# Performance work log

Measured on AMD Instinct MI355X. Metric: run time of the kernel, lower is better.

The kernel has to match this reference:

```python
import jax, jax.numpy as jnp
import numpy as np

B, S, D, H = 4, 2048, 256, 8
HD = D // H
SCALE = float(np.sqrt(HD))  # temperature = head_dim ** 0.5


def setup_inputs() -> dict:
    key = jax.random.key(0)
    ks = jax.random.split(key, 12)
    w = lambda k, shape: jax.random.normal(k, shape, dtype=jnp.float32) * 0.05
    x = jax.random.normal(ks[0], (B, S, D), dtype=jnp.float32)
    adj = jax.random.randint(ks[1], (B, S, S), 0, 2, dtype=jnp.int32)
    return {
        "x": x,
        "adj": adj,
        "w_qkv": w(ks[2], (3 * D, D)),
        "b_qkv": jnp.zeros((3 * D,), jnp.float32),
        "ln_g": jnp.ones((D,), jnp.float32),
        "ln_b": jnp.zeros((D,), jnp.float32),
        "w_fc": w(ks[3], (D, D)),
        "b_fc": jnp.zeros((D,), jnp.float32),
        "w_z": w(ks[4], (D, D)),
        "b_z": jnp.full((D,), -2.0, jnp.float32),  # init_bias fills w_z bias with -2
        "u_z": w(ks[5], (D, D)),
        "w_r": w(ks[6], (D, D)),
        "u_r": w(ks[7], (D, D)),
        "w_g": w(ks[8], (D, D)),
        "u_g": w(ks[9], (D, D)),
    }


def reference(x, adj, w_qkv, b_qkv, ln_g, ln_b, w_fc, b_fc,
              w_z, b_z, u_z, w_r, u_r, w_g, u_g):
    residual = x
    # LayerNorm (eps=1e-5, torch default)
    mu = jnp.mean(x, axis=-1, keepdims=True)
    var = jnp.var(x, axis=-1, keepdims=True)
    xn = (x - mu) / jnp.sqrt(var + 1e-5) * ln_g + ln_b
    # fused QKV projection -> (B*H, S, 3*HD), batch-major over (b, h)
    qkv = xn @ w_qkv.T + b_qkv                       # [B,S,3D]
    qkv = qkv.reshape(B, S, H, 3 * HD).transpose(0, 2, 1, 3).reshape(B * H, S, 3 * HD)
    q, k, v = jnp.split(qkv, 3, axis=-1)
    # masked scaled dot-product attention (full NxN scores, as in original)
    attn = jnp.einsum('nqd,nkd->nqk', q, k) / SCALE  # [B*H,S,S]
    adj_r = jnp.repeat(adj, H, axis=0)               # batch-major, matches attn layout
    attn = jnp.where(adj_r == 0, -jnp.inf, attn)
    attn = jax.nn.softmax(attn, axis=-1)
    out = jnp.einsum('nqk,nkd->nqd', attn, v)        # [B*H,S,HD]
    # Faithful replication of torch's view(n_head, batch, ...) applied to
    # batch-major data (an ordering quirk in the original module).
    out = out.reshape(H, B, S, HD).transpose(1, 2, 0, 3).reshape(B, S, D)
    y = jax.nn.relu(out @ w_fc.T + b_fc)
    # GRU gate: x=residual, y=attention branch
    z = jax.nn.sigmoid(y @ w_z.T + b_z + residual @ u_z.T)
    r = jax.nn.sigmoid(y @ w_r.T + residual @ u_r.T)
    h_hat = jnp.tanh(y @ w_g.T + (r * residual) @ u_g.T)
    return (1.0 - z) * residual + z * h_hat
```

## Files before the change

### kernel.cpp

```cpp
#include <hip/hip_runtime.h>
#include <hip/hip_bf16.h>
#include <math.h>

#define B_  4
#define S_  2048
#define D_  256
#define H_  8
#define HD_ 32
#define QSCALE 0.25504175929589786f

typedef short  bf16x8 __attribute__((ext_vector_type(8)));
typedef float  f32x4  __attribute__((ext_vector_type(4)));
typedef float  f32x16 __attribute__((ext_vector_type(16)));
typedef unsigned short ushort_t;
typedef unsigned int   uint_t;

__device__ __forceinline__ ushort_t f2b(float f) {
    union { float f; unsigned u; } v; v.f = f;
    unsigned r = (v.u + 0x7FFFu + ((v.u >> 16) & 1u)) >> 16;
    return (ushort_t)r;
}
__device__ __forceinline__ float b2f(ushort_t s) {
    return __uint_as_float((uint_t)s << 16);
}
__device__ __forceinline__ f32x16 zero16() {
    f32x16 z;
#pragma unroll
    for (int i = 0; i < 16; ++i) z[i] = 0.f;
    return z;
}
__device__ __forceinline__ float wave_allsum(float v) {
#pragma unroll
    for (int o = 32; o > 0; o >>= 1) v += __shfl_xor(v, o, 64);
    return v;
}

#define WQ_SZ 196608
#define WS_SZ 65536
#define NB_WQ  48
#define NB_LN4 2048
__global__ __launch_bounds__(256)
void prep_kernel(const float* __restrict__ w0, ushort_t* __restrict__ wout,
                 const float* __restrict__ x, const float* __restrict__ g,
                 const float* __restrict__ bb, ushort_t* __restrict__ xn_b) {
    __shared__ float T[16][260];
    int blk = blockIdx.x, tid = threadIdx.x;
    if (blk < NB_WQ) {
        int ct = blk;
#pragma unroll
        for (int p = 0; p < 4; ++p) {
            int u = p * 256 + tid;
            int row = u >> 6, col = (u & 63) * 4;
            float4 v = *(const float4*)(w0 + (size_t)(ct * 16 + row) * 256 + col);
            T[row][col]     = v.x; T[row][col + 1] = v.y;
            T[row][col + 2] = v.z; T[row][col + 3] = v.w;
        }
        __syncthreads();
        ushort_t* ob = wout + (size_t)blk * 4096;
#pragma unroll
        for (int p = 0; p < 2; ++p) {
            int m = p * 256 + tid;
            int l = m & 15, qd = (m >> 4) & 3, ks = m >> 6;
            const float* tp = &T[l][ks * 32 + qd * 8];
            union { ushort_t u[8]; uint4 q; } pk;
#pragma unroll
            for (int j = 0; j < 8; ++j) pk.u[j] = f2b(tp[j]);
            *(uint4*)(ob + ks * 512 + qd * 128 + l * 8) = pk.q;
        }
    } else {
        int wave = tid >> 6, lane = tid & 63;
        int row = (blk - NB_WQ) * 4 + wave;
        int col = lane * 4;
        float4 t = *(const float4*)(x + (size_t)row * 256 + col);
        float s = wave_allsum(t.x + t.y + t.z + t.w);
        float mu = s * (1.0f / D_);
        float d0 = t.x - mu, d1 = t.y - mu, d2 = t.z - mu, d3 = t.w - mu;
        float v = wave_allsum(d0 * d0 + d1 * d1 + d2 * d2 + d3 * d3);
        float rstd = rsqrtf(v * (1.0f / D_) + 1e-5f);
        float4 gv = *(const float4*)(g + col);
        float4 bv = *(const float4*)(bb + col);
        union { ushort_t u[4]; uint2 q; } o;
        o.u[0] = f2b(d0 * rstd * gv.x + bv.x);
        o.u[1] = f2b(d1 * rstd * gv.y + bv.y);
        o.u[2] = f2b(d2 * rstd * gv.z + bv.z);
        o.u[3] = f2b(d3 * rstd * gv.w + bv.w);
        *(uint2*)(xn_b + (size_t)row * 256 + col) = o.q;
    }
}

__global__ __launch_bounds__(256)
void gemm_qkv(const ushort_t* __restrict__ A, const ushort_t* __restrict__ Wf,
              const float* __restrict__ bias, ushort_t* __restrict__ outb,
              ushort_t* __restrict__ vT, ushort_t* __restrict__ kD,
              const int* __restrict__ adj, uint_t* __restrict__ bits) {
    __shared__ ushort_t Sa[64][264];
    int tid = threadIdx.x;
    int bid = blockIdx.x;
    int grp = bid / 19, r = bid - grp * 19;
    if (r >= 3) {
        int a = grp * 16 + (r - 3);
        int b = a >> 11, q = a & 2047;
        const int4* arow = (const int4*)(adj + (size_t)a * 2048);
        int4 v0 = arow[tid * 2];
        int4 v1 = arow[tid * 2 + 1];
        unsigned byte = (unsigned)(v0.x != 0)        | ((unsigned)(v0.y != 0) << 1)
                      | ((unsigned)(v0.z != 0) << 2) | ((unsigned)(v0.w != 0) << 3)
                      | ((unsigned)(v1.x != 0) << 4) | ((unsigned)(v1.y != 0) << 5)
                      | ((unsigned)(v1.z != 0) << 6) | ((unsigned)(v1.w != 0) << 7);
        unsigned char* lb = (unsigned char*)&Sa[0][0];
        lb[tid] = (unsigned char)byte;
        __syncthreads();
        if (tid < 64) {
            uint_t w = *(const uint_t*)&lb[tid * 4];
            bits[((size_t)b * 64 + tid) * 2048 + q] = w;
        }
        return;
    }
    int gidx = grp * 3 + r;
    int m0 = (gidx / 12) * 64, n0 = (gidx % 12) * 64;

    int wave = tid >> 6, lane = tid & 63, l = lane & 15, quad = lane >> 4;
    int wm = wave >> 1, wn = wave & 1;
    {
#pragma unroll
        for (int j = 0; j < 8; ++j) {
            int u = tid + j * 256;
            int row = u >> 5, c = (u & 31) * 8;
            *(uint4*)&Sa[row][c] = *(const uint4*)(A + (size_t)(m0 + row) * 256 + c);
        }
    }
    __syncthreads();

    bf16x8 af[2][8];
#pragma unroll
    for (int mt = 0; mt < 2; ++mt)
#pragma unroll
        for (int ks = 0; ks < 8; ++ks)
            af[mt][ks] = *(const bf16x8*)&Sa[wm * 32 + mt * 16 + l][ks * 32 + quad * 8];

    f32x4 acc[2][2];
#pragma unroll
    for (int i = 0; i < 2; ++i)
#pragma unroll
        for (int j = 0; j < 2; ++j) acc[i][j] = (f32x4){0.f, 0.f, 0.f, 0.f};

#pragma unroll
    for (int nt = 0; nt < 2; ++nt) {
        int ct = (n0 >> 4) + wn * 2 + nt;
        bf16x8 wfr[8];
#pragma unroll
        for (int ks = 0; ks < 8; ++ks)
            wfr[ks] = *(const bf16x8*)(Wf + (((size_t)ct * 8 + ks) * 64 + lane) * 8);
#pragma unroll
        for (int ks = 0; ks < 8; ++ks) {
            acc[0][nt] = __builtin_amdgcn_mfma_f32_16x16x32_bf16(af[0][ks], wfr[ks], acc[0][nt], 0, 0, 0);
            acc[1][nt] = __builtin_amdgcn_mfma_f32_16x16x32_bf16(af[1][ks], wfr[ks], acc[1][nt], 0, 0, 0);
        }
    }

    __syncthreads();
    ushort_t* So = &Sa[0][0];
#pragma unroll
    for (int nt = 0; nt < 2; ++nt) {
        int col = wn * 32 + nt * 16 + l;
        int gcol = n0 + col;
        float bv = bias[gcol];
        float qs = ((gcol % 96) < 32) ? QSCALE : 1.0f;
#pragma unroll
        for (int mt = 0; mt < 2; ++mt)
#pragma unroll
            for (int r2 = 0; r2 < 4; ++r2) {
                int row = wm * 32 + mt * 16 + quad * 4 + r2;
                So[row * 72 + col] = f2b((acc[mt][nt][r2] + bv) * qs);
            }
    }
    __syncthreads();
    {
        int row = tid >> 2, seg = tid & 3;
        uint4 v0 = *(uint4*)&So[row * 72 + seg * 16];
        uint4 v1 = *(uint4*)&So[row * 72 + seg * 16 + 8];
        ushort_t* op = outb + (size_t)(m0 + row) * 768 + n0 + seg * 16;
        ((uint4*)op)[0] = v0;
        ((uint4*)op)[1] = v1;
    }

    int vs = n0 % 96;

    if (vs != 64) {
        int kloc = (vs == 0) ? 32 : 0;
        int h  = (vs == 0) ? (n0 / 96) : ((n0 - 32) / 96);
        int b  = m0 >> 11;
        int s0 = m0 & (S_ - 1);
        int krow = tid >> 2, kd = (tid & 3) * 8;
        uint4 v = *(uint4*)&So[krow * 72 + kloc + kd];
        *(uint4*)&kD[((size_t)(b * 8 + h) * S_ + s0 + krow) * 32 + kd] = v;
    }

    if (vs != 0) {
        int vloc = (vs == 64) ? 0 : 32;
        int h  = (n0 + vloc) / 96;
        int b  = m0 >> 11;
        int s0 = m0 & (S_ - 1);
        ushort_t* vstage = &Sa[0][0] + 8192;
        {
            int c = tid & 31, seg = tid >> 5;
            ushort_t tmp[8];
#pragma unroll
            for (int i = 0; i < 8; ++i)
                tmp[i] = So[(seg * 8 + i) * 72 + vloc + c];
            uint_t u[4];
#pragma unroll
            for (int i = 0; i < 4; ++i)
                u[i] = (uint_t)tmp[2 * i] | ((uint_t)tmp[2 * i + 1] << 16);
            *(uint4*)&vstage[c * 72 + seg * 8] = make_uint4(u[0], u[1], u[2], u[3]);
        }
        __syncthreads();
        {
            int d = tid >> 3, tseg = tid & 7;
            uint4 v = *(uint4*)&vstage[d * 72 + tseg * 8];
            *(uint4*)&vT[((size_t)(b * 8 + h) * 32 + d) * S_ + s0 + tseg * 8] = v;
        }
    }
}

__global__ __launch_bounds__(512)
void fused_gate(const ushort_t* __restrict__ attn_b, const float* __restrict__ xf,
                const ushort_t* __restrict__ wfc, const ushort_t* __restrict__ wz,
                const ushort_t* __restrict__ uz, const ushort_t* __restrict__ wr,
                const ushort_t* __restrict__ ur, const ushort_t* __restrict__ wg,
                const ushort_t* __restrict__ ug, const float* __restrict__ bfc,
                const float* __restrict__ bz, float* __restrict__ out) {
    __shared__ ushort_t Sa[32][264];
    __shared__ ushort_t Sx[32][264];
    __shared__ ushort_t Sy[32][264];
    auto St = Sa;
    int tid = threadIdx.x;
    int wave = tid >> 6, lane = tid & 63, l = lane & 15, quad = lane >> 4;
    int m0 = blockIdx.x * 32;
    int colbase = wave * 32;

    {
        int row = tid >> 4, c0 = (tid & 15) * 16;
        const ushort_t* ap = attn_b + (size_t)(m0 + row) * 256 + c0;
        uint4 a0 = ((const uint4*)ap)[0];
        uint4 a1 = ((const uint4*)ap)[1];
        *(uint4*)&Sa[row][c0] = a0;
        *(uint4*)&Sa[row][c0 + 8] = a1;
        const float4* xp = (const float4*)(xf + (size_t)(m0 + row) * 256 + c0);
        float4 f0 = xp[0], f1 = xp[1], f2_ = xp[2], f3 = xp[3];
        union { __hip_bfloat162 h[4]; uint4 u; } p0, p1;
        p0.h[0] = __float22bfloat162_rn(make_float2(f0.x, f0.y));
        p0.h[1] = __float22bfloat162_rn(make_float2(f0.z, f0.w));
        p0.h[2] = __float22bfloat162_rn(make_float2(f1.x, f1.y));
        p0.h[3] = __float22bfloat162_rn(make_float2(f1.z, f1.w));
        p1.h[0] = __float22bfloat162_rn(make_float2(f2_.x, f2_.y));
        p1.h[1] = __float22bfloat162_rn(make_float2(f2_.z, f2_.w));
        p1.h[2] = __float22bfloat162_rn(make_float2(f3.x, f3.y));
        p1.h[3] = __float22bfloat162_rn(make_float2(f3.z, f3.w));
        *(uint4*)&Sx[row][c0]     = p0.u;
        *(uint4*)&Sx[row][c0 + 8] = p1.u;
    }
    __syncthreads();

    {
        f32x4 ya[2][2];
#pragma unroll
        for (int mt = 0; mt < 2; ++mt)
#pragma unroll
            for (int nt = 0; nt < 2; ++nt) ya[mt][nt] = (f32x4){0.f, 0.f, 0.f, 0.f};
#pragma unroll
        for (int nt = 0; nt < 2; ++nt) {
            size_t fb = ((size_t)(wave * 2 + nt) * 8) * 512 + lane * 8;
#pragma unroll
            for (int ks = 0; ks < 8; ++ks) {
                bf16x8 wfr = *(const bf16x8*)(wfc + fb + ks * 512);
                bf16x8 a0 = *(const bf16x8*)&Sa[l][ks * 32 + quad * 8];
                bf16x8 a1 = *(const bf16x8*)&Sa[16 + l][ks * 32 + quad * 8];
                ya[0][nt] = __builtin_amdgcn_mfma_f32_16x16x32_bf16(a0, wfr, ya[0][nt], 0, 0, 0);
                ya[1][nt] = __builtin_amdgcn_mfma_f32_16x16x32_bf16(a1, wfr, ya[1][nt], 0, 0, 0);
            }
        }
        __syncthreads();
#pragma unroll
        for (int nt = 0; nt < 2; ++nt) {
            int col = colbase + nt * 16 + l;
            float bv = bfc[col];
#pragma unroll
            for (int mt = 0; mt < 2; ++mt)
#pragma unroll
                for (int r = 0; r < 4; ++r)
                    Sy[mt * 16 + quad * 4 + r][col] = f2b(fmaxf(ya[mt][nt][r] + bv, 0.0f));
        }
    }
    __syncthreads();

    f32x4 az[2][2], ar[2][2], ag[2][2];
#pragma unroll
    for (int mt = 0; mt < 2; ++mt)
#pragma unroll
        for (int nt = 0; nt < 2; ++nt) {
            az[mt][nt] = (f32x4){0.f, 0.f, 0.f, 0.f};
            ar[mt][nt] = (f32x4){0.f, 0.f, 0.f, 0.f};
            ag[mt][nt] = (f32x4){0.f, 0.f, 0.f, 0.f};
        }
#pragma unroll
    for (int nt = 0; nt < 2; ++nt) {
        size_t fb = ((size_t)(wave * 2 + nt) * 8) * 512 + lane * 8;
#pragma unroll
        for (int ks = 0; ks < 8; ++ks) {
            bf16x8 fz  = *(const bf16x8*)(wz + fb + ks * 512);
            bf16x8 fuz = *(const bf16x8*)(uz + fb + ks * 512);
            bf16x8 fr  = *(const bf16x8*)(wr + fb + ks * 512);
            bf16x8 fur = *(const bf16x8*)(ur + fb + ks * 512);
            bf16x8 fg  = *(const bf16x8*)(wg + fb + ks * 512);
            bf16x8 fy0 = *(const bf16x8*)&Sy[l][ks * 32 + quad * 8];
            bf16x8 fy1 = *(const bf16x8*)&Sy[16 + l][ks * 32 + quad * 8];
            bf16x8 fx0 = *(const bf16x8*)&Sx[l][ks * 32 + quad * 8];
            bf16x8 fx1 = *(const bf16x8*)&Sx[16 + l][ks * 32 + quad * 8];
            az[0][nt] = __builtin_amdgcn_mfma_f32_16x16x32_bf16(fy0, fz,  az[0][nt], 0, 0, 0);
            az[0][nt] = __builtin_amdgcn_mfma_f32_16x16x32_bf16(fx0, fuz, az[0][nt], 0, 0, 0);
            az[1][nt] = __builtin_amdgcn_mfma_f32_16x16x32_bf16(fy1, fz,  az[1][nt], 0, 0, 0);
            az[1][nt] = __builtin_amdgcn_mfma_f32_16x16x32_bf16(fx1, fuz, az[1][nt], 0, 0, 0);
            ar[0][nt] = __builtin_amdgcn_mfma_f32_16x16x32_bf16(fy0, fr,  ar[0][nt], 0, 0, 0);
            ar[0][nt] = __builtin_amdgcn_mfma_f32_16x16x32_bf16(fx0, fur, ar[0][nt], 0, 0, 0);
            ar[1][nt] = __builtin_amdgcn_mfma_f32_16x16x32_bf16(fy1, fr,  ar[1][nt], 0, 0, 0);
            ar[1][nt] = __builtin_amdgcn_mfma_f32_16x16x32_bf16(fx1, fur, ar[1][nt], 0, 0, 0);
            ag[0][nt] = __builtin_amdgcn_mfma_f32_16x16x32_bf16(fy0, fg,  ag[0][nt], 0, 0, 0);
            ag[1][nt] = __builtin_amdgcn_mfma_f32_16x16x32_bf16(fy1, fg,  ag[1][nt], 0, 0, 0);
        }
    }
#pragma unroll
    for (int nt = 0; nt < 2; ++nt) {
        int col = colbase + nt * 16 + l;
        float bzv = bz[col];
#pragma unroll
        for (int mt = 0; mt < 2; ++mt)
#pragma unroll
            for (int r = 0; r < 4; ++r) {
                int row = mt * 16 + quad * 4 + r;
                az[mt][nt][r] = 1.0f / (1.0f + __expf(-(az[mt][nt][r] + bzv)));
                float rr  = 1.0f / (1.0f + __expf(-ar[mt][nt][r]));
                St[row][col] = f2b(rr * b2f(Sx[row][col]));
            }
    }
    __syncthreads();

    f32x4 fcc[2][2];
#pragma unroll
    for (int mt = 0; mt < 2; ++mt)
#pragma unroll
        for (int nt = 0; nt < 2; ++nt) fcc[mt][nt] = (f32x4){0.f, 0.f, 0.f, 0.f};
#pragma unroll
    for (int nt = 0; nt < 2; ++nt) {
        size_t fb = ((size_t)(wave * 2 + nt) * 8) * 512 + lane * 8;
#pragma unroll
        for (int ks = 0; ks < 8; ++ks) {
            bf16x8 fu  = *(const bf16x8*)(ug + fb + ks * 512);
            bf16x8 ft0 = *(const bf16x8*)&St[l][ks * 32 + quad * 8];
            bf16x8 ft1 = *(const bf16x8*)&St[16 + l][ks * 32 + quad * 8];
            fcc[0][nt] = __builtin_amdgcn_mfma_f32_16x16x32_bf16(ft0, fu, fcc[0][nt], 0, 0, 0);
            fcc[1][nt] = __builtin_amdgcn_mfma_f32_16x16x32_bf16(ft1, fu, fcc[1][nt], 0, 0, 0);
        }
    }
#pragma unroll
    for (int nt = 0; nt < 2; ++nt) {
        int col = colbase + nt * 16 + l;
#pragma unroll
        for (int mt = 0; mt < 2; ++mt)
#pragma unroll
            for (int r = 0; r < 4; ++r) {
                int row = mt * 16 + quad * 4 + r;
                float v = ag[mt][nt][r] + fcc[mt][nt][r];
                float e = __expf(2.0f * v);
                float h = 1.0f - 2.0f / (e + 1.0f);
                float zz = az[mt][nt][r];
                size_t idx = (size_t)(m0 + row) * 256 + col;
                out[idx] = (1.0f - zz) * xf[idx] + zz * h;
            }
    }
}

#define ATTN_COMPUTE(CUR, A0, A1)                                                         \
    {                                                                                     \
        _Pragma("unroll")                                                                 \
        for (int kb2 = 0; kb2 < 2; ++kb2) {                                               \
            const int kb = kofs + kb2 * 32;                                               \
            bf16x8 kf1 = *(const bf16x8*)&Ks[CUR][kb + lane5][(hi ^ b3) * 8];             \
            bf16x8 kf2 = *(const bf16x8*)&Ks[CUR][kb + lane5][((2 + hi) ^ b3) * 8];       \
            f32x16 sc = zero16();                                                         \
            sc = __builtin_amdgcn_mfma_f32_32x32x16_bf16(kf1, qf1, sc, 0, 0, 0);          \
            sc = __builtin_amdgcn_mfma_f32_32x32x16_bf16(kf2, qf2, sc, 0, 0, 0);          \
            uint_t wsub = (kb2 ? (A1) : (A0)) >> hsh8;                                    \
            union { uint_t u[8]; bf16x8 v[2]; } pp;                                       \
            _Pragma("unroll")                                                             \
            for (int i = 0; i < 8; ++i) {                                                 \
                const int c = 2 * i + ((i >> 2) * 8);                                     \
                float e0 = __builtin_amdgcn_exp2f(sc[2 * i]);                             \
                float e1 = __builtin_amdgcn_exp2f(sc[2 * i + 1]);                         \
                uint_t mm0 = (uint_t)((int)(wsub << (31 - c)) >> 31);                     \
                uint_t mm1 = (uint_t)((int)(wsub << (30 - c)) >> 31);                     \
                e0 = __uint_as_float(__float_as_uint(e0) & mm0);                          \
                e1 = __uint_as_float(__float_as_uint(e1) & mm1);                          \
                union { __hip_bfloat162 b2; uint_t u; } p;                                \
                p.b2 = __float22bfloat162_rn(make_float2(e0, e1));                        \
                pp.u[i] = p.u;                                                            \
            }                                                                             \
            bf16x8 vb1 = *(const bf16x8*)&Vt[CUR][lane5][kb + hsh8];                      \
            bf16x8 vb2 = *(const bf16x8*)&Vt[CUR][lane5][kb + 16 + hsh8];                 \
            __builtin_amdgcn_s_setprio(1);                                                \
            oacc  = __builtin_amdgcn_mfma_f32_32x32x16_bf16(pp.v[0], vb1,  oacc,  0, 0, 0); \
            aones = __builtin_amdgcn_mfma_f32_32x32x16_bf16(pp.v[0], ones, aones, 0, 0, 0); \
            oacc  = __builtin_amdgcn_mfma_f32_32x32x16_bf16(pp.v[1], vb2,  oacc,  0, 0, 0); \
            aones = __builtin_amdgcn_mfma_f32_32x32x16_bf16(pp.v[1], ones, aones, 0, 0, 0); \
            __builtin_amdgcn_s_setprio(0);                                                \
        }                                                                                 \
    }

__global__ __launch_bounds__(256)
void attn_kernel(const ushort_t* __restrict__ qkvb, const ushort_t* __restrict__ kD,
                 const ushort_t* __restrict__ vT,
                 const uint_t* __restrict__ abits, ushort_t* __restrict__ attn_b,
                 const float* __restrict__ gw0, const float* __restrict__ gw1,
                 const float* __restrict__ gw2, const float* __restrict__ gw3,
                 const float* __restrict__ gw4, const float* __restrict__ gw5,
                 const float* __restrict__ gw6, ushort_t* __restrict__ wout) {
    __shared__ ushort_t Ks[2][128][40];
    __shared__ ushort_t Vt[2][32][136];

    int tid = threadIdx.x;
    int lid = blockIdx.x;

    if (lid >= 1024) {
        int wblk = lid - 1024;
        int seg = wblk >> 4, ct = wblk & 15;
        const float* src = (seg == 0) ? gw0 : (seg == 1) ? gw1 : (seg == 2) ? gw2 :
                           (seg == 3) ? gw3 : (seg == 4) ? gw4 : (seg == 5) ? gw5 : gw6;
        float* T = (float*)&Ks[0][0][0];
#pragma unroll
        for (int p = 0; p < 4; ++p) {
            int u = p * 256 + tid;
            int row = u >> 6, col = (u & 63) * 4;
            float4 v = *(const float4*)(src + (size_t)(ct * 16 + row) * 256 + col);
            T[row * 260 + col]     = v.x; T[row * 260 + col + 1] = v.y;
            T[row * 260 + col + 2] = v.z; T[row * 260 + col + 3] = v.w;
        }
        __syncthreads();
        ushort_t* ob = wout + (size_t)(48 + wblk) * 4096;
#pragma unroll
        for (int p = 0; p < 2; ++p) {
            int m = p * 256 + tid;
            int l2 = m & 15, qd = (m >> 4) & 3, ks2 = m >> 6;
            const float* tp = &T[l2 * 260 + ks2 * 32 + qd * 8];
            union { ushort_t u[8]; uint4 q; } pk;
#pragma unroll
            for (int j = 0; j < 8; ++j) pk.u[j] = f2b(tp[j]);
            *(uint4*)(ob + ks2 * 512 + qd * 128 + l2 * 8) = pk.q;
        }
        return;
    }

    int wave = tid >> 6, lane = tid & 63;
    int lane5 = lane & 31, hi = lane >> 5;
    int hsh8 = hi * 8;
    int pair = wave >> 1, half = wave & 1;

    int L   = (lid & 7) * 128 + (lid >> 3);
    int q0  = (L & 31) * 64;
    int n   = L >> 5;
    int b = n >> 3, h = n & 7;
    int bp = n & 3, hp = n >> 2;

    const ushort_t* base = qkvb + (size_t)b * S_ * 768 + h * 96;
    int qbase = pair * 32;
    int myq = q0 + qbase + lane5;
    const int kofs = half * 64;

    bf16x8 qf1 = *(const bf16x8*)(base + (size_t)myq * 768 + hsh8);
    bf16x8 qf2 = *(const bf16x8*)(base + (size_t)myq * 768 + 16 + hsh8);

    bf16x8 ones;
#pragma unroll
    for (int i = 0; i < 8; ++i) ones[i] = (short)0x3F80;

    f32x16 oacc = zero16(), aones = zero16();

    int skey = tid >> 1, sj = tid & 1;
    int prow = (skey & ~12) | ((skey & 4) << 1) | ((skey & 8) >> 1);
    int pxor = ((prow >> 3) & 1) << 3;
    int vd = tid >> 3, vk = (tid & 7) * 8;
    const ushort_t* vptr = vT + ((size_t)n * 32 + vd) * S_ + vk;
    const ushort_t* kpt  = kD + ((size_t)n * S_ + skey) * 32 + sj * 16;
    const uint_t* tb = abits + ((size_t)b * 64) * 2048 + myq;

    uint_t aw0 = tb[(size_t)(half * 2 + 0) * 2048];
    uint_t aw1 = tb[(size_t)(half * 2 + 1) * 2048];
    {
        uint4 ka = *(const uint4*)(kpt);
        uint4 kb_ = *(const uint4*)(kpt + 8);
        uint4 va = *(const uint4*)(vptr);
        uint4 vb_ = *(const uint4*)(vptr + 64);
        *(uint4*)&Ks[0][prow][(sj * 16 + 0) ^ pxor] = ka;
        *(uint4*)&Ks[0][prow][(sj * 16 + 8) ^ pxor] = kb_;
        *(uint4*)&Vt[0][vd][vk] = va;
        *(uint4*)&Vt[0][vd][vk + 64] = vb_;
    }
    uint4 kv0 = *(const uint4*)(kpt + (size_t)128 * 32);
    uint4 kv1 = *(const uint4*)(kpt + (size_t)128 * 32 + 8);
    uint4 vv0 = *(const uint4*)(vptr + 128);
    uint4 vv1 = *(const uint4*)(vptr + 192);
    __syncthreads();

    int b3 = (lane >> 3) & 1;

#pragma unroll 1
    for (int w = 0; w < 15; ++w) {
        int k0 = w * 128;
        int cur = w & 1;
        *(uint4*)&Ks[cur ^ 1][prow][(sj * 16 + 0) ^ pxor] = kv0;
        *(uint4*)&Ks[cur ^ 1][prow][(sj * 16 + 8) ^ pxor] = kv1;
        *(uint4*)&Vt[cur ^ 1][vd][vk] = vv0;
        *(uint4*)&Vt[cur ^ 1][vd][vk + 64] = vv1;
        int wn = ((k0 + 128) >> 5) + half * 2;
        uint_t awn0 = tb[(size_t)(wn + 0) * 2048];
        uint_t awn1 = tb[(size_t)(wn + 1) * 2048];
        int kpre = (k0 + 256) & (S_ - 1);
        kv0 = *(const uint4*)(kpt + (size_t)kpre * 32);
        kv1 = *(const uint4*)(kpt + (size_t)kpre * 32 + 8);
        vv0 = *(const uint4*)(vptr + kpre);
        vv1 = *(const uint4*)(vptr + kpre + 64);

        ATTN_COMPUTE(cur, aw0, aw1)

        aw0 = awn0; aw1 = awn1;
        __syncthreads();
    }
    ATTN_COMPUTE(1, aw0, aw1)
    __syncthreads();

    float* red = (float*)&Ks[0][0][0];
    if (half) {
        float* dst = red + pair * 2048 + lane * 4;
#pragma unroll
        for (int j = 0; j < 4; ++j) {
            f32x4 t;
            t[0] = oacc[4 * j]; t[1] = oacc[4 * j + 1];
            t[2] = oacc[4 * j + 2]; t[3] = oacc[4 * j + 3];
            *(f32x4*)(dst + j * 256) = t;
        }
#pragma unroll
        for (int j = 0; j < 4; ++j) {
            f32x4 t;
            t[0] = aones[4 * j]; t[1] = aones[4 * j + 1];
            t[2] = aones[4 * j + 2]; t[3] = aones[4 * j + 3];
            *(f32x4*)(dst + (4 + j) * 256) = t;
        }
    }
    __syncthreads();
    if (!half) {
        const float* src = red + pair * 2048 + lane * 4;
#pragma unroll
        for (int j = 0; j < 4; ++j) {
            f32x4 t = *(const f32x4*)(src + j * 256);
            oacc[4 * j] += t[0]; oacc[4 * j + 1] += t[1];
            oacc[4 * j + 2] += t[2]; oacc[4 * j + 3] += t[3];
        }
#pragma unroll
        for (int j = 0; j < 4; ++j) {
            f32x4 t = *(const f32x4*)(src + (4 + j) * 256);
            aones[4 * j] += t[0]; aones[4 * j + 1] += t[1];
            aones[4 * j + 2] += t[2]; aones[4 * j + 3] += t[3];
        }
    }
    __syncthreads();

    ushort_t* Ost = &Ks[0][0][0];
    if (!half) {
#pragma unroll
        for (int r = 0; r < 16; ++r) {
            int qr = (r & 3) + 8 * (r >> 2) + 4 * hi;
            Ost[(qbase + qr) * 40 + lane5] = f2b(oacc[r] / aones[r]);
        }
    }
    __syncthreads();
    {
        int row = tid >> 2, part = tid & 3;
        uint4 v = *(uint4*)&Ost[row * 40 + part * 8];
        *(uint4*)&attn_b[((size_t)(bp * S_ + q0 + row)) * 256 + hp * 32 + part * 8] = v;
    }
}

extern "C" void kernel_launch(void* const* d_in, const int* in_sizes, int n_in,
                              void* d_out, int out_size, void* d_ws, size_t ws_size,
                              hipStream_t stream) {
    const float* x     = (const float*)d_in[0];
    const int*   adj   = (const int*)d_in[1];
    const float* w_qkv = (const float*)d_in[2];
    const float* b_qkv = (const float*)d_in[3];
    const float* ln_g  = (const float*)d_in[4];
    const float* ln_b  = (const float*)d_in[5];
    const float* w_fc  = (const float*)d_in[6];
    const float* b_fc  = (const float*)d_in[7];
    const float* w_z   = (const float*)d_in[8];
    const float* b_z   = (const float*)d_in[9];
    const float* u_z   = (const float*)d_in[10];
    const float* w_r   = (const float*)d_in[11];
    const float* u_r   = (const float*)d_in[12];
    const float* w_g   = (const float*)d_in[13];
    const float* u_g   = (const float*)d_in[14];
    float* out = (float*)d_out;

    const size_t TOK  = (size_t)B_ * S_;
    const size_t TOKD = TOK * D_;
    ushort_t* xn_b   = (ushort_t*)d_ws;
    ushort_t* qkv_b  = xn_b + TOKD;
    ushort_t* attn_b = qkv_b + TOK * 768;
    ushort_t* wb     = attn_b + TOKD;
    uint_t*   bits   = (uint_t*)(wb + WQ_SZ + 7 * WS_SZ);
    ushort_t* vTb    = (ushort_t*)(bits + (size_t)B_ * S_ * S_ / 32);
    ushort_t* kDb    = vTb + (size_t)32 * 32 * S_;

    ushort_t* wq_b  = wb;
    ushort_t* wfc_b = wb + WQ_SZ;
    ushort_t* wz_b  = wfc_b + WS_SZ;
    ushort_t* uz_b  = wz_b + WS_SZ;
    ushort_t* wr_b  = uz_b + WS_SZ;
    ushort_t* ur_b  = wr_b + WS_SZ;
    ushort_t* wg_b  = ur_b + WS_SZ;
    ushort_t* ug_b  = wg_b + WS_SZ;

    prep_kernel<<<NB_WQ + NB_LN4, 256, 0, stream>>>(
        w_qkv, wb, x, ln_g, ln_b, xn_b);

    gemm_qkv<<<9728, 256, 0, stream>>>(xn_b, wq_b, b_qkv, qkv_b, vTb, kDb, adj, bits);

    attn_kernel<<<1136, 256, 0, stream>>>(qkv_b, kDb, vTb, bits, attn_b,
                                          w_fc, w_z, u_z, w_r, u_r, w_g, u_g, wb);

    fused_gate<<<256, 512, 0, stream>>>(
        attn_b, x, wfc_b, wz_b, uz_b, wr_b, ur_b, wg_b, ug_b, b_fc, b_z, out);
}
```

Before: 208.7 us.

## Batch adj bit-packing per block and widen fused_gate to 16 waves

Adjacency packing blocks in the QKV GEMM launch now each handle 64 query rows instead of one. They transpose the packed bytes through shared memory and write coalesced uint4 words, which shrinks the grid from 9728 to 1664 blocks and cuts per-block overhead. fused_gate goes from 512 to 1024 threads, with each wave owning one 16-column tile instead of two, so there is more parallelism across the 256 blocks. The risks are lower per-wave ILP, higher register pressure at 1024 threads, and fewer, longer-running packing blocks.

```diff
diff --git a/kernel.cpp b/kernel.cpp
--- a/kernel.cpp
+++ b/kernel.cpp
@@ -96,27 +96,38 @@
     __shared__ ushort_t Sa[64][264];
     int tid = threadIdx.x;
     int bid = blockIdx.x;
-    int grp = bid / 19, r = bid - grp * 19;
-    if (r >= 3) {
-        int a = grp * 16 + (r - 3);
-        int b = a >> 11, q = a & 2047;
-        const int4* arow = (const int4*)(adj + (size_t)a * 2048);
-        int4 v0 = arow[tid * 2];
-        int4 v1 = arow[tid * 2 + 1];
-        unsigned byte = (unsigned)(v0.x != 0)        | ((unsigned)(v0.y != 0) << 1)
-                      | ((unsigned)(v0.z != 0) << 2) | ((unsigned)(v0.w != 0) << 3)
-                      | ((unsigned)(v1.x != 0) << 4) | ((unsigned)(v1.y != 0) << 5)
-                      | ((unsigned)(v1.z != 0) << 6) | ((unsigned)(v1.w != 0) << 7);
+    int grp = bid / 13, r = bid - grp * 13;
+    if (r == 12) {
+        int a = grp;
+        int ab = a >> 5, q0 = (a & 31) * 64;
         unsigned char* lb = (unsigned char*)&Sa[0][0];
-        lb[tid] = (unsigned char)byte;
+#pragma unroll 4
+        for (int rr = 0; rr < 64; ++rr) {
+            const int4* p = (const int4*)(adj + ((size_t)ab * 2048 + q0 + rr) * 2048);
+            int4 v0 = p[tid * 2];
+            int4 v1 = p[tid * 2 + 1];
+            unsigned byte = (unsigned)(v0.x != 0)        | ((unsigned)(v0.y != 0) << 1)
+                          | ((unsigned)(v0.z != 0) << 2) | ((unsigned)(v0.w != 0) << 3)
+                          | ((unsigned)(v1.x != 0) << 4) | ((unsigned)(v1.y != 0) << 5)
+                          | ((unsigned)(v1.z != 0) << 6) | ((unsigned)(v1.w != 0) << 7);
+            lb[rr * 260 + tid] = (unsigned char)byte;
+        }
         __syncthreads();
-        if (tid < 64) {
-            uint_t w = *(const uint_t*)&lb[tid * 4];
-            bits[((size_t)b * 64 + tid) * 2048 + q] = w;
+        {
+            int w = tid >> 2, qq = (tid & 3) * 16;
+            uint_t wd[16];
+#pragma unroll
+            for (int j = 0; j < 16; ++j)
+                wd[j] = *(const uint_t*)&lb[(qq + j) * 260 + w * 4];
+            uint_t* dst = bits + ((size_t)ab * 64 + w) * 2048 + q0 + qq;
+#pragma unroll
+            for (int c = 0; c < 4; ++c)
+                *(uint4*)(dst + c * 4) = make_uint4(wd[4 * c], wd[4 * c + 1],
+                                                   wd[4 * c + 2], wd[4 * c + 3]);
         }
         return;
     }
-    int gidx = grp * 3 + r;
+    int gidx = grp * 12 + r;
     int m0 = (gidx / 12) * 64, n0 = (gidx % 12) * 64;
 
     int wave = tid >> 6, lane = tid & 63, l = lane & 15, quad = lane >> 4;
@@ -223,7 +234,7 @@
     }
 }
 
-__global__ __launch_bounds__(512)
+__global__ __launch_bounds__(1024)
 void fused_gate(const ushort_t* __restrict__ attn_b, const float* __restrict__ xf,
                 const ushort_t* __restrict__ wfc, const ushort_t* __restrict__ wz,
                 const ushort_t* __restrict__ uz, const ushort_t* __restrict__ wr,
@@ -237,147 +248,112 @@
     int tid = threadIdx.x;
     int wave = tid >> 6, lane = tid & 63, l = lane & 15, quad = lane >> 4;
     int m0 = blockIdx.x * 32;
-    int colbase = wave * 32;
+    int col = wave * 16 + l;
 
     {
-        int row = tid >> 4, c0 = (tid & 15) * 16;
+        int row = tid >> 5, c0 = (tid & 31) * 8;
         const ushort_t* ap = attn_b + (size_t)(m0 + row) * 256 + c0;
-        uint4 a0 = ((const uint4*)ap)[0];
-        uint4 a1 = ((const uint4*)ap)[1];
-        *(uint4*)&Sa[row][c0] = a0;
-        *(uint4*)&Sa[row][c0 + 8] = a1;
+        *(uint4*)&Sa[row][c0] = *((const uint4*)ap);
         const float4* xp = (const float4*)(xf + (size_t)(m0 + row) * 256 + c0);
-        float4 f0 = xp[0], f1 = xp[1], f2_ = xp[2], f3 = xp[3];
-        union { __hip_bfloat162 h[4]; uint4 u; } p0, p1;
+        float4 f0 = xp[0], f1 = xp[1];
+        union { __hip_bfloat162 h[4]; uint4 u; } p0;
         p0.h[0] = __float22bfloat162_rn(make_float2(f0.x, f0.y));
         p0.h[1] = __float22bfloat162_rn(make_float2(f0.z, f0.w));
         p0.h[2] = __float22bfloat162_rn(make_float2(f1.x, f1.y));
         p0.h[3] = __float22bfloat162_rn(make_float2(f1.z, f1.w));
-        p1.h[0] = __float22bfloat162_rn(make_float2(f2_.x, f2_.y));
-        p1.h[1] = __float22bfloat162_rn(make_float2(f2_.z, f2_.w));
-        p1.h[2] = __float22bfloat162_rn(make_float2(f3.x, f3.y));
-        p1.h[3] = __float22bfloat162_rn(make_float2(f3.z, f3.w));
-        *(uint4*)&Sx[row][c0]     = p0.u;
-        *(uint4*)&Sx[row][c0 + 8] = p1.u;
-    }
-    __syncthreads();
-
+        *(uint4*)&Sx[row][c0] = p0.u;
+    }
+    __syncthreads();
+
+    size_t fb = (size_t)(wave * 8) * 512 + lane * 8;
     {
-        f32x4 ya[2][2];
+        f32x4 ya[2];
+        ya[0] = (f32x4){0.f, 0.f, 0.f, 0.f};
+        ya[1] = (f32x4){0.f, 0.f, 0.f, 0.f};
+#pragma unroll
+        for (int ks = 0; ks < 8; ++ks) {
+            bf16x8 wfr = *(const bf16x8*)(wfc + fb + ks * 512);
+            bf16x8 a0 = *(const bf16x8*)&Sa[l][ks * 32 + quad * 8];
+            bf16x8 a1 = *(const bf16x8*)&Sa[16 + l][ks * 32 + quad * 8];
+            ya[0] = __builtin_amdgcn_mfma_f32_16x16x32_bf16(a0, wfr, ya[0], 0, 0, 0);
+            ya[1] = __builtin_amdgcn_mfma_f32_16x16x32_bf16(a1, wfr, ya[1], 0, 0, 0);
+        }
+        __syncthreads();
+        float bv = bfc[col];
 #pragma unroll
         for (int mt = 0; mt < 2; ++mt)
 #pragma unroll
-            for (int nt = 0; nt < 2; ++nt) ya[mt][nt] = (f32x4){0.f, 0.f, 0.f, 0.f};
-#pragma unroll
-        for (int nt = 0; nt < 2; ++nt) {
-            size_t fb = ((size_t)(wave * 2 + nt) * 8) * 512 + lane * 8;
-#pragma unroll
-            for (int ks = 0; ks < 8; ++ks) {
-                bf16x8 wfr = *(const bf16x8*)(wfc + fb + ks * 512);
-                bf16x8 a0 = *(const bf16x8*)&Sa[l][ks * 32 + quad * 8];
-                bf16x8 a1 = *(const bf16x8*)&Sa[16 + l][ks * 32 + quad * 8];
-                ya[0][nt] = __builtin_amdgcn_mfma_f32_16x16x32_bf16(a0, wfr, ya[0][nt], 0, 0, 0);
-                ya[1][nt] = __builtin_amdgcn_mfma_f32_16x16x32_bf16(a1, wfr, ya[1][nt], 0, 0, 0);
-            }
-        }
-        __syncthreads();
-#pragma unroll
-        for (int nt = 0; nt < 2; ++nt) {
-            int col = colbase + nt * 16 + l;
-            float bv = bfc[col];
-#pragma unroll
-            for (int mt = 0; mt < 2; ++mt)
-#pragma unroll
-                for (int r = 0; r < 4; ++r)
-                    Sy[mt * 16 + quad * 4 + r][col] = f2b(fmaxf(ya[mt][nt][r] + bv, 0.0f));
-        }
-    }
-    __syncthreads();
-
-    f32x4 az[2][2], ar[2][2], ag[2][2];
-#pragma unroll
-    for (int mt = 0; mt < 2; ++mt)
-#pragma unroll
-        for (int nt = 0; nt < 2; ++nt) {
-            az[mt][nt] = (f32x4){0.f, 0.f, 0.f, 0.f};
-            ar[mt][nt] = (f32x4){0.f, 0.f, 0.f, 0.f};
-            ag[mt][nt] = (f32x4){0.f, 0.f, 0.f, 0.f};
-        }
-#pragma unroll
-    for (int nt = 0; nt < 2; ++nt) {
-        size_t fb = ((size_t)(wave * 2 + nt) * 8) * 512 + lane * 8;
-#pragma unroll
-        for (int ks = 0; ks < 8; ++ks) {
-            bf16x8 fz  = *(const bf16x8*)(wz + fb + ks * 512);
-            bf16x8 fuz = *(const bf16x8*)(uz + fb + ks * 512);
-            bf16x8 fr  = *(const bf16x8*)(wr + fb + ks * 512);
-            bf16x8 fur = *(const bf16x8*)(ur + fb + ks * 512);
-            bf16x8 fg  = *(const bf16x8*)(wg + fb + ks * 512);
-            bf16x8 fy0 = *(const bf16x8*)&Sy[l][ks * 32 + quad * 8];
-            bf16x8 fy1 = *(const bf16x8*)&Sy[16 + l][ks * 32 + quad * 8];
-            bf16x8 fx0 = *(const bf16x8*)&Sx[l][ks * 32 + quad * 8];
-            bf16x8 fx1 = *(const bf16x8*)&Sx[16 + l][ks * 32 + quad * 8];
-            az[0][nt] = __builtin_amdgcn_mfma_f32_16x16x32_bf16(fy0, fz,  az[0][nt], 0, 0, 0);
-            az[0][nt] = __builtin_amdgcn_mfma_f32_16x16x32_bf16(fx0, fuz, az[0][nt], 0, 0, 0);
-            az[1][nt] = __builtin_amdgcn_mfma_f32_16x16x32_bf16(fy1, fz,  az[1][nt], 0, 0, 0);
-            az[1][nt] = __builtin_amdgcn_mfma_f32_16x16x32_bf16(fx1, fuz, az[1][nt], 0, 0, 0);
-            ar[0][nt] = __builtin_amdgcn_mfma_f32_16x16x32_bf16(fy0, fr,  ar[0][nt], 0, 0, 0);
-            ar[0][nt] = __builtin_amdgcn_mfma_f32_16x16x32_bf16(fx0, fur, ar[0][nt], 0, 0, 0);
-            ar[1][nt] = __builtin_amdgcn_mfma_f32_16x16x32_bf16(fy1, fr,  ar[1][nt], 0, 0, 0);
-            ar[1][nt] = __builtin_amdgcn_mfma_f32_16x16x32_bf16(fx1, fur, ar[1][nt], 0, 0, 0);
-            ag[0][nt] = __builtin_amdgcn_mfma_f32_16x16x32_bf16(fy0, fg,  ag[0][nt], 0, 0, 0);
-            ag[1][nt] = __builtin_amdgcn_mfma_f32_16x16x32_bf16(fy1, fg,  ag[1][nt], 0, 0, 0);
-        }
-    }
-#pragma unroll
-    for (int nt = 0; nt < 2; ++nt) {
-        int col = colbase + nt * 16 + l;
+            for (int r = 0; r < 4; ++r)
+                Sy[mt * 16 + quad * 4 + r][col] = f2b(fmaxf(ya[mt][r] + bv, 0.0f));
+    }
+    __syncthreads();
+
+    f32x4 az[2], ar[2], ag[2];
+#pragma unroll
+    for (int mt = 0; mt < 2; ++mt) {
+        az[mt] = (f32x4){0.f, 0.f, 0.f, 0.f};
+        ar[mt] = (f32x4){0.f, 0.f, 0.f, 0.f};
+        ag[mt] = (f32x4){0.f, 0.f, 0.f, 0.f};
+    }
+#pragma unroll
+    for (int ks = 0; ks < 8; ++ks) {
+        bf16x8 fz  = *(const bf16x8*)(wz + fb + ks * 512);
+        bf16x8 fuz = *(const bf16x8*)(uz + fb + ks * 512);
+        bf16x8 fr  = *(const bf16x8*)(wr + fb + ks * 512);
+        bf16x8 fur = *(const bf16x8*)(ur + fb + ks * 512);
+        bf16x8 fg  = *(const bf16x8*)(wg + fb + ks * 512);
+        bf16x8 fy0 = *(const bf16x8*)&Sy[l][ks * 32 + quad * 8];
+        bf16x8 fy1 = *(const bf16x8*)&Sy[16 + l][ks * 32 + quad * 8];
+        bf16x8 fx0 = *(const bf16x8*)&Sx[l][ks * 32 + quad * 8];
+        bf16x8 fx1 = *(const bf16x8*)&Sx[16 + l][ks * 32 + quad * 8];
+        az[0] = __builtin_amdgcn_mfma_f32_16x16x32_bf16(fy0, fz,  az[0], 0, 0, 0);
+        az[0] = __builtin_amdgcn_mfma_f32_16x16x32_bf16(fx0, fuz, az[0], 0, 0, 0);
+        az[1] = __builtin_amdgcn_mfma_f32_16x16x32_bf16(fy1, fz,  az[1], 0, 0, 0);
+        az[1] = __builtin_amdgcn_mfma_f32_16x16x32_bf16(fx1, fuz, az[1], 0, 0, 0);
+        ar[0] = __builtin_amdgcn_mfma_f32_16x16x32_bf16(fy0, fr,  ar[0], 0, 0, 0);
+        ar[0] = __builtin_amdgcn_mfma_f32_16x16x32_bf16(fx0, fur, ar[0], 0, 0, 0);
+        ar[1] = __builtin_amdgcn_mfma_f32_16x16x32_bf16(fy1, fr,  ar[1], 0, 0, 0);
+        ar[1] = __builtin_amdgcn_mfma_f32_16x16x32_bf16(fx1, fur, ar[1], 0, 0, 0);
+        ag[0] = __builtin_amdgcn_mfma_f32_16x16x32_bf16(fy0, fg,  ag[0], 0, 0, 0);
+        ag[1] = __builtin_amdgcn_mfma_f32_16x16x32_bf16(fy1, fg,  ag[1], 0, 0, 0);
+    }
+    {
         float bzv = bz[col];
 #pragma unroll
         for (int mt = 0; mt < 2; ++mt)
 #pragma unroll
             for (int r = 0; r < 4; ++r) {
                 int row = mt * 16 + quad * 4 + r;
-                az[mt][nt][r] = 1.0f / (1.0f + __expf(-(az[mt][nt][r] + bzv)));
-                float rr  = 1.0f / (1.0f + __expf(-ar[mt][nt][r]));
+                az[mt][r] = 1.0f / (1.0f + __expf(-(az[mt][r] + bzv)));
+                float rr  = 1.0f / (1.0f + __expf(-ar[mt][r]));
                 St[row][col] = f2b(rr * b2f(Sx[row][col]));
             }
     }
     __syncthreads();
 
-    f32x4 fcc[2][2];
+    f32x4 fcc[2];
+    fcc[0] = (f32x4){0.f, 0.f, 0.f, 0.f};
+    fcc[1] = (f32x4){0.f, 0.f, 0.f, 0.f};
+#pragma unroll
+    for (int ks = 0; ks < 8; ++ks) {
+        bf16x8 fu  = *(const bf16x8*)(ug + fb + ks * 512);
+        bf16x8 ft0 = *(const bf16x8*)&St[l][ks * 32 + quad * 8];
+        bf16x8 ft1 = *(const bf16x8*)&St[16 + l][ks * 32 + quad * 8];
+        fcc[0] = __builtin_amdgcn_mfma_f32_16x16x32_bf16(ft0, fu, fcc[0], 0, 0, 0);
+        fcc[1] = __builtin_amdgcn_mfma_f32_16x16x32_bf16(ft1, fu, fcc[1], 0, 0, 0);
+    }
 #pragma unroll
     for (int mt = 0; mt < 2; ++mt)
 #pragma unroll
-        for (int nt = 0; nt < 2; ++nt) fcc[mt][nt] = (f32x4){0.f, 0.f, 0.f, 0.f};
-#pragma unroll
-    for (int nt = 0; nt < 2; ++nt) {
-        size_t fb = ((size_t)(wave * 2 + nt) * 8) * 512 + lane * 8;
-#pragma unroll
-        for (int ks = 0; ks < 8; ++ks) {
-            bf16x8 fu  = *(const bf16x8*)(ug + fb + ks * 512);
-            bf16x8 ft0 = *(const bf16x8*)&St[l][ks * 32 + quad * 8];
-            bf16x8 ft1 = *(const bf16x8*)&St[16 + l][ks * 32 + quad * 8];
-            fcc[0][nt] = __builtin_amdgcn_mfma_f32_16x16x32_bf16(ft0, fu, fcc[0][nt], 0, 0, 0);
-            fcc[1][nt] = __builtin_amdgcn_mfma_f32_16x16x32_bf16(ft1, fu, fcc[1][nt], 0, 0, 0);
-        }
-    }
-#pragma unroll
-    for (int nt = 0; nt < 2; ++nt) {
-        int col = colbase + nt * 16 + l;
-#pragma unroll
-        for (int mt = 0; mt < 2; ++mt)
-#pragma unroll
-            for (int r = 0; r < 4; ++r) {
-                int row = mt * 16 + quad * 4 + r;
-                float v = ag[mt][nt][r] + fcc[mt][nt][r];
-                float e = __expf(2.0f * v);
-                float h = 1.0f - 2.0f / (e + 1.0f);
-                float zz = az[mt][nt][r];
-                size_t idx = (size_t)(m0 + row) * 256 + col;
-                out[idx] = (1.0f - zz) * xf[idx] + zz * h;
-            }
-    }
+        for (int r = 0; r < 4; ++r) {
+            int row = mt * 16 + quad * 4 + r;
+            float v = ag[mt][r] + fcc[mt][r];
+            float e = __expf(2.0f * v);
+            float h = 1.0f - 2.0f / (e + 1.0f);
+            float zz = az[mt][r];
+            size_t idx = (size_t)(m0 + row) * 256 + col;
+            out[idx] = (1.0f - zz) * xf[idx] + zz * h;
+        }
 }
 
 #define ATTN_COMPUTE(CUR, A0, A1)                                                         \
@@ -631,11 +607,11 @@
     prep_kernel<<<NB_WQ + NB_LN4, 256, 0, stream>>>(
         w_qkv, wb, x, ln_g, ln_b, xn_b);
 
-    gemm_qkv<<<9728, 256, 0, stream>>>(xn_b, wq_b, b_qkv, qkv_b, vTb, kDb, adj, bits);
+    gemm_qkv<<<1664, 256, 0, stream>>>(xn_b, wq_b, b_qkv, qkv_b, vTb, kDb, adj, bits);
 
     attn_kernel<<<1136, 256, 0, stream>>>(qkv_b, kDb, vTb, bits, attn_b,
                                           w_fc, w_z, u_z, w_r, u_r, w_g, u_g, wb);
 
-    fused_gate<<<256, 512, 0, stream>>>(
+    fused_gate<<<256, 1024, 0, stream>>>(
         attn_b, x, wfc_b, wz_b, uz_b, wr_b, ur_b, wg_b, ug_b, b_fc, b_z, out);
 }
```

Result: no change. 212.7 us (+1.9%).
